# Kernel tuning notes

Hardware: AMD Instinct MI355X
Metric: run time of the kernel (lower is better)

Reference implementation:

```python
import jax, jax.numpy as jnp
import numpy as np

MARGIN = 0.05

def setup_inputs() -> dict:
    key = jax.random.key(0)
    k1, k2 = jax.random.split(key)
    N, D = 8192, 1024
    x = jax.random.normal(k1, (N, D), dtype=jnp.float32)
    y = jax.random.normal(k2, (N, D), dtype=jnp.float32)
    # cosine-style embeddings: L2 normalize
    x = x / jnp.linalg.norm(x, axis=1, keepdims=True)
    y = y / jnp.linalg.norm(y, axis=1, keepdims=True)
    return {"x": x, "y": y}

def reference(x, y):
    N = x.shape[0]
    # positive similarity per pair: [N]
    pos_sim = jnp.sum(x * y, axis=1)
    # hard-negative mining (no gradient through mining)
    xs = jax.lax.stop_gradient(x)
    ys = jax.lax.stop_gradient(y)
    sim = xs @ ys.T  # [N, N]
    diag = jnp.eye(N, dtype=bool)
    diff_neg = (jax.lax.stop_gradient(pos_sim)[:, None] - sim) < 0.0
    masked = jnp.where(diag | diff_neg, jnp.float32(-1.0), sim)
    neg_idx = jnp.argmax(masked, axis=1)  # [N] int
    # negative similarity (gradients flow through x and gathered y rows)
    neg_sim = jnp.sum(x * y[neg_idx], axis=1)
    loss = jnp.mean(jax.nn.relu(MARGIN - pos_sim + neg_sim))
    return loss
```

## Files before the change

kernel.cpp:

```cpp
#include <hip/hip_runtime.h>

#define NROWS 8192
#define DDIM  1024
#define BM 128
#define BN 128
#define BKB 128
#define NSTRIPES 16
#define CT_PER_STRIPE 4
#define MARGIN_F 0.05f
#define FP8_SCALE 8.0f

typedef __attribute__((ext_vector_type(8)))  int   int8v;
typedef __attribute__((ext_vector_type(4)))  int   int4v;
typedef __attribute__((ext_vector_type(16))) float floatx16;

__device__ __forceinline__ void g2lds16(const void* g, void* l) {
  __builtin_amdgcn_global_load_lds(
      (const __attribute__((address_space(1))) void*)g,
      (__attribute__((address_space(3))) void*)l, 16, 0, 0);
}

__device__ __forceinline__ unsigned long long pack_key(float v, int j) {
  unsigned int u = __float_as_uint(v);
  u = (u & 0x80000000u) ? ~u : (u | 0x80000000u);
  return ((unsigned long long)u << 32) | (unsigned long long)(0x7FFFFFFFu - (unsigned int)j);
}

__global__ void prep_kernel(const float* __restrict__ x, const float* __restrict__ y,
                            unsigned int* __restrict__ xq, unsigned int* __restrict__ yq,
                            float* __restrict__ pos, unsigned long long* __restrict__ keys,
                            float* __restrict__ out) {
  const int row = blockIdx.x;
  const int t = threadIdx.x;
  const float4 a = ((const float4*)(x + (size_t)row * DDIM))[t];
  const float4 b = ((const float4*)(y + (size_t)row * DDIM))[t];
  float s = a.x * b.x + a.y * b.y + a.z * b.z + a.w * b.w;

  int pa = __builtin_amdgcn_cvt_pk_fp8_f32(a.x * FP8_SCALE, a.y * FP8_SCALE, 0, false);
  pa     = __builtin_amdgcn_cvt_pk_fp8_f32(a.z * FP8_SCALE, a.w * FP8_SCALE, pa, true);
  int pb = __builtin_amdgcn_cvt_pk_fp8_f32(b.x * FP8_SCALE, b.y * FP8_SCALE, 0, false);
  pb     = __builtin_amdgcn_cvt_pk_fp8_f32(b.z * FP8_SCALE, b.w * FP8_SCALE, pb, true);
  xq[(size_t)row * 256 + t] = (unsigned int)pa;
  yq[(size_t)row * 256 + t] = (unsigned int)pb;

  for (int m = 32; m; m >>= 1) s += __shfl_down(s, m, 64);
  __shared__ float ps[4];
  if ((t & 63) == 0) ps[t >> 6] = s;
  __syncthreads();
  if (t == 0) {
    pos[row] = ps[0] + ps[1] + ps[2] + ps[3];
    keys[row] = 0ULL;
    if (row == 0) out[0] = 0.f;
  }
}

__global__ __launch_bounds__(256, 2) void mine_kernel(
    const unsigned char* __restrict__ xq, const unsigned char* __restrict__ yq,
    const float* __restrict__ pos, unsigned long long* __restrict__ keys) {
  __shared__ unsigned char As[BM * BKB];
  __shared__ unsigned char Bs[BN * BKB];
  __shared__ float pos_s[BM];

  const int t = threadIdx.x;
  const int rowBase = blockIdx.x * BM;
  const int stripe  = blockIdx.y;
  if (t < BM) pos_s[t] = pos[rowBase + t] * (FP8_SCALE * FP8_SCALE);

  const int lane = t & 63;
  const int wave = t >> 6;
  const int r31  = lane & 31;
  const int kh   = lane >> 5;
  const int fragBase = r31 * BKB + (((2 * kh) ^ (r31 & 7)) << 4);
  const int offA = wave * (32 * BKB) + fragBase;

  for (int ct = 0; ct < CT_PER_STRIPE; ++ct) {
    const int colBase = stripe * (BN * CT_PER_STRIPE) + ct * BN;

    floatx16 acc[4];
#pragma unroll
    for (int ni = 0; ni < 4; ++ni)
#pragma unroll
      for (int r = 0; r < 16; ++r) acc[ni][r] = 0.f;

    for (int k0 = 0; k0 < DDIM; k0 += BKB) {
      __syncthreads();
#pragma unroll
      for (int i = 0; i < 4; ++i) {
        const int c  = i * 256 + t;
        const int r  = c >> 3;
        const int sw = (c & 7) ^ (r & 7);
        const unsigned char* gA = xq + (size_t)(rowBase + r) * DDIM + k0 + sw * 16;
        const unsigned char* gB = yq + (size_t)(colBase + r) * DDIM + k0 + sw * 16;
        unsigned char* lA = &As[(size_t)(i * 256 + wave * 64) * 16];
        unsigned char* lB = &Bs[(size_t)(i * 256 + wave * 64) * 16];
        g2lds16(gA, lA);
        g2lds16(gB, lB);
      }
      __syncthreads();

#pragma unroll
      for (int ks = 0; ks < 2; ++ks) {
        const int kx = ks << 6;
        int4v alo = *(const int4v*)&As[offA ^ kx];
        int4v ahi = *(const int4v*)&As[(offA ^ kx) ^ 16];
        int8v af = __builtin_shufflevector(alo, ahi, 0, 1, 2, 3, 4, 5, 6, 7);
#pragma unroll
        for (int ni = 0; ni < 4; ++ni) {
          const int offB = ni * (32 * BKB) + fragBase;
          int4v blo = *(const int4v*)&Bs[offB ^ kx];
          int4v bhi = *(const int4v*)&Bs[(offB ^ kx) ^ 16];
          int8v bf = __builtin_shufflevector(blo, bhi, 0, 1, 2, 3, 4, 5, 6, 7);
          acc[ni] = __builtin_amdgcn_mfma_scale_f32_32x32x64_f8f6f4(
              af, bf, acc[ni], 0, 0,
              0, 0x7F7F7F7F,
              0, 0x7F7F7F7F);
        }
      }
    }

#pragma unroll
    for (int reg = 0; reg < 16; ++reg) {
      const int row_l = 32 * wave + (reg & 3) + 8 * (reg >> 2) + 4 * kh;
      const int row_g = rowBase + row_l;
      const float p = pos_s[row_l];
      float bestv = -1.0e30f; int bestj = 0;
#pragma unroll
      for (int ni = 0; ni < 4; ++ni) {
        float v = acc[ni][reg];
        const int col_g = colBase + 32 * ni + r31;
        if (col_g == row_g || v > p) v = -1024.0f;
        if (v > bestv || (v == bestv && col_g < bestj)) { bestv = v; bestj = col_g; }
      }
      unsigned long long key = pack_key(bestv, bestj);
#pragma unroll
      for (int m = 1; m <= 16; m <<= 1) {
        unsigned long long o = __shfl_xor(key, m, 64);
        if (o > key) key = o;
      }
      if (r31 == 0) atomicMax(&keys[row_g], key);
    }
  }
}

__global__ void final_kernel(const float* __restrict__ x, const float* __restrict__ y,
                             const float* __restrict__ pos,
                             const unsigned long long* __restrict__ keys,
                             float* __restrict__ out) {
  const int t = threadIdx.x;
  const int lane = t & 63, wave = t >> 6;
  float accl = 0.f;
#pragma unroll
  for (int i = 0; i < 8; ++i) {
    const int row = blockIdx.x * 32 + i * 4 + wave;
    const unsigned long long k = keys[row];
    const int j = 0x7FFFFFFF - (int)(k & 0xFFFFFFFFULL);
    const float4* xr = (const float4*)(x + (size_t)row * DDIM);
    const float4* yr = (const float4*)(y + (size_t)j * DDIM);
    float s = 0.f;
#pragma unroll
    for (int u = 0; u < 4; ++u) {
      const float4 a = xr[lane + 64 * u];
      const float4 b = yr[lane + 64 * u];
      s += a.x * b.x + a.y * b.y + a.z * b.z + a.w * b.w;
    }
    for (int m = 32; m; m >>= 1) s += __shfl_down(s, m, 64);
    if (lane == 0) {
      const float l = MARGIN_F - pos[row] + s;
      accl += l > 0.f ? l : 0.f;
    }
  }
  __shared__ float ps[4];
  if (lane == 0) ps[wave] = accl;
  __syncthreads();
  if (t == 0) atomicAdd(out, (ps[0] + ps[1] + ps[2] + ps[3]) * (1.0f / (float)NROWS));
}

extern "C" void kernel_launch(void* const* d_in, const int* in_sizes, int n_in,
                              void* d_out, int out_size, void* d_ws, size_t ws_size,
                              hipStream_t stream) {
  const float* x = (const float*)d_in[0];
  const float* y = (const float*)d_in[1];
  float* out = (float*)d_out;

  unsigned long long* keys = (unsigned long long*)d_ws;
  float* pos = (float*)((char*)d_ws + (size_t)NROWS * 8);
  unsigned char* xq = (unsigned char*)d_ws + (size_t)NROWS * 8 + (size_t)NROWS * 4;
  unsigned char* yq = xq + (size_t)NROWS * DDIM;

  prep_kernel<<<NROWS, 256, 0, stream>>>(x, y, (unsigned int*)xq, (unsigned int*)yq,
                                         pos, keys, out);
  dim3 grid(NROWS / BM, NSTRIPES);
  mine_kernel<<<grid, 256, 0, stream>>>(xq, yq, pos, keys);
  final_kernel<<<NROWS / 32, 256, 0, stream>>>(x, y, pos, keys, out);
}
```

Measured before the change: 236.8 us.

## Enlarge mining tile to 128x256 with 2x2 wave layout for more fragment reuse

Doubles the column tile of the FP8 similarity GEMM from 128 to 256 and halves the number of column stripes. Waves are rearranged into a 2x2 grid, each computing a 64x128 sub-tile with two A fragments reused across four B fragments. This raises the MFMA-to-LDS-load ratio and cuts redundant global reloads of A. In exchange it doubles accumulator registers (128 floats per lane), grows LDS use to 48KB per block, and halves the grid size, which may hurt occupancy given launch_bounds(256,2).

```diff
diff --git a/kernel.cpp b/kernel.cpp
--- a/kernel.cpp
+++ b/kernel.cpp
@@ -3,9 +3,9 @@
 #define NROWS 8192
 #define DDIM  1024
 #define BM 128
-#define BN 128
+#define BN 256
 #define BKB 128
-#define NSTRIPES 16
+#define NSTRIPES 8
 #define CT_PER_STRIPE 4
 #define MARGIN_F 0.05f
 #define FP8_SCALE 8.0f
@@ -68,19 +68,23 @@
 
   const int lane = t & 63;
   const int wave = t >> 6;
+  const int wr = wave >> 1, wc = wave & 1;
   const int r31  = lane & 31;
   const int kh   = lane >> 5;
-  const int fragBase = r31 * BKB + (((2 * kh) ^ (r31 & 7)) << 4);
-  const int offA = wave * (32 * BKB) + fragBase;
+  const int fragOff = ((2 * kh) ^ (r31 & 7)) << 4;
+  const int offA0 = (64 * wr + r31) * BKB + fragOff;
+  const int offB0 = (128 * wc + r31) * BKB + fragOff;
 
   for (int ct = 0; ct < CT_PER_STRIPE; ++ct) {
     const int colBase = stripe * (BN * CT_PER_STRIPE) + ct * BN;
 
-    floatx16 acc[4];
-#pragma unroll
-    for (int ni = 0; ni < 4; ++ni)
-#pragma unroll
-      for (int r = 0; r < 16; ++r) acc[ni][r] = 0.f;
+    floatx16 acc[2][4];
+#pragma unroll
+    for (int mi = 0; mi < 2; ++mi)
+#pragma unroll
+      for (int ni = 0; ni < 4; ++ni)
+#pragma unroll
+        for (int r = 0; r < 16; ++r) acc[mi][ni][r] = 0.f;
 
     for (int k0 = 0; k0 < DDIM; k0 += BKB) {
       __syncthreads();
@@ -89,55 +93,67 @@
         const int c  = i * 256 + t;
         const int r  = c >> 3;
         const int sw = (c & 7) ^ (r & 7);
-        const unsigned char* gA = xq + (size_t)(rowBase + r) * DDIM + k0 + sw * 16;
-        const unsigned char* gB = yq + (size_t)(colBase + r) * DDIM + k0 + sw * 16;
-        unsigned char* lA = &As[(size_t)(i * 256 + wave * 64) * 16];
-        unsigned char* lB = &Bs[(size_t)(i * 256 + wave * 64) * 16];
-        g2lds16(gA, lA);
-        g2lds16(gB, lB);
+        g2lds16(xq + (size_t)(rowBase + r) * DDIM + k0 + sw * 16,
+                &As[(size_t)(i * 256 + wave * 64) * 16]);
+      }
+#pragma unroll
+      for (int i = 0; i < 8; ++i) {
+        const int c  = i * 256 + t;
+        const int r  = c >> 3;
+        const int sw = (c & 7) ^ (r & 7);
+        g2lds16(yq + (size_t)(colBase + r) * DDIM + k0 + sw * 16,
+                &Bs[(size_t)(i * 256 + wave * 64) * 16]);
       }
       __syncthreads();
 
 #pragma unroll
       for (int ks = 0; ks < 2; ++ks) {
         const int kx = ks << 6;
-        int4v alo = *(const int4v*)&As[offA ^ kx];
-        int4v ahi = *(const int4v*)&As[(offA ^ kx) ^ 16];
-        int8v af = __builtin_shufflevector(alo, ahi, 0, 1, 2, 3, 4, 5, 6, 7);
+        int8v af[2];
+#pragma unroll
+        for (int mi = 0; mi < 2; ++mi) {
+          const int oA = (offA0 + mi * 32 * BKB) ^ kx;
+          int4v lo = *(const int4v*)&As[oA];
+          int4v hi = *(const int4v*)&As[oA ^ 16];
+          af[mi] = __builtin_shufflevector(lo, hi, 0, 1, 2, 3, 4, 5, 6, 7);
+        }
 #pragma unroll
         for (int ni = 0; ni < 4; ++ni) {
-          const int offB = ni * (32 * BKB) + fragBase;
-          int4v blo = *(const int4v*)&Bs[offB ^ kx];
-          int4v bhi = *(const int4v*)&Bs[(offB ^ kx) ^ 16];
+          const int oB = (offB0 + ni * 32 * BKB) ^ kx;
+          int4v blo = *(const int4v*)&Bs[oB];
+          int4v bhi = *(const int4v*)&Bs[oB ^ 16];
           int8v bf = __builtin_shufflevector(blo, bhi, 0, 1, 2, 3, 4, 5, 6, 7);
-          acc[ni] = __builtin_amdgcn_mfma_scale_f32_32x32x64_f8f6f4(
-              af, bf, acc[ni], 0, 0,
-              0, 0x7F7F7F7F,
-              0, 0x7F7F7F7F);
-        }
-      }
-    }
-
-#pragma unroll
-    for (int reg = 0; reg < 16; ++reg) {
-      const int row_l = 32 * wave + (reg & 3) + 8 * (reg >> 2) + 4 * kh;
-      const int row_g = rowBase + row_l;
-      const float p = pos_s[row_l];
-      float bestv = -1.0e30f; int bestj = 0;
-#pragma unroll
-      for (int ni = 0; ni < 4; ++ni) {
-        float v = acc[ni][reg];
-        const int col_g = colBase + 32 * ni + r31;
-        if (col_g == row_g || v > p) v = -1024.0f;
-        if (v > bestv || (v == bestv && col_g < bestj)) { bestv = v; bestj = col_g; }
-      }
-      unsigned long long key = pack_key(bestv, bestj);
-#pragma unroll
-      for (int m = 1; m <= 16; m <<= 1) {
-        unsigned long long o = __shfl_xor(key, m, 64);
-        if (o > key) key = o;
-      }
-      if (r31 == 0) atomicMax(&keys[row_g], key);
+          acc[0][ni] = __builtin_amdgcn_mfma_scale_f32_32x32x64_f8f6f4(
+              af[0], bf, acc[0][ni], 0, 0, 0, 0x7F7F7F7F, 0, 0x7F7F7F7F);
+          acc[1][ni] = __builtin_amdgcn_mfma_scale_f32_32x32x64_f8f6f4(
+              af[1], bf, acc[1][ni], 0, 0, 0, 0x7F7F7F7F, 0, 0x7F7F7F7F);
+        }
+      }
+    }
+
+#pragma unroll
+    for (int mi = 0; mi < 2; ++mi) {
+#pragma unroll
+      for (int reg = 0; reg < 16; ++reg) {
+        const int row_l = 64 * wr + 32 * mi + (reg & 3) + 8 * (reg >> 2) + 4 * kh;
+        const int row_g = rowBase + row_l;
+        const float p = pos_s[row_l];
+        float bestv = -1.0e30f; int bestj = 0;
+#pragma unroll
+        for (int ni = 0; ni < 4; ++ni) {
+          float v = acc[mi][ni][reg];
+          const int col_g = colBase + 128 * wc + 32 * ni + r31;
+          if (col_g == row_g || v > p) v = -1024.0f;
+          if (v > bestv || (v == bestv && col_g < bestj)) { bestv = v; bestj = col_g; }
+        }
+        unsigned long long key = pack_key(bestv, bestj);
+#pragma unroll
+        for (int m = 1; m <= 16; m <<= 1) {
+          unsigned long long o = __shfl_xor(key, m, 64);
+          if (o > key) key = o;
+        }
+        if (r31 == 0) atomicMax(&keys[row_g], key);
+      }
     }
   }
 }
```

Result: faster. 221.7 us (-6.4%).
